# Kernel tuning notes

Hardware: AMD Instinct MI355X
Metric: run time of the kernel (lower is better)

The kernel has to match this reference:

```python
import jax, jax.numpy as jnp
import numpy as np

D_MODEL = 256; D_FFN = 1024; N_LEVELS = 4; N_HEADS = 8; N_POINTS = 4; N_VT = 8
D_HEAD = D_MODEL // N_HEADS
SHAPES = [(64, 64), (32, 32), (16, 16), (8, 8)]
L_SP = sum(h * w for h, w in SHAPES)  # 5440
BATCH = 4
EPS = 1e-5


def _ln(x, g, b):
    m = jnp.mean(x, -1, keepdims=True)
    xc = x - m
    v = jnp.mean(xc * xc, -1, keepdims=True)
    return g * xc * jax.lax.rsqrt(v + EPS) + b


def _bilinear(v_flat, x, y, H, W):
    # v_flat: (N, H*W, M, Dh); x, y: (N, Q, M) pixel coords (align_corners=False, zero padding)
    x0 = jnp.floor(x); y0 = jnp.floor(y)
    wx = x - x0; wy = y - y0
    out = 0.0
    for cx, cy, w in ((x0, y0, (1 - wx) * (1 - wy)), (x0 + 1, y0, wx * (1 - wy)),
                      (x0, y0 + 1, (1 - wx) * wy), (x0 + 1, y0 + 1, wx * wy)):
        valid = (cx >= 0) & (cx < W) & (cy >= 0) & (cy < H)
        xi = jnp.clip(cx, 0, W - 1).astype(jnp.int32)
        yi = jnp.clip(cy, 0, H - 1).astype(jnp.int32)
        idx = (yi * W + xi)[..., None]  # (N, Q, M, 1)
        g = jnp.take_along_axis(v_flat, idx, axis=1)  # (N, Q, M, Dh)
        out = out + (w * valid)[..., None] * g
    return out


def _msdeform_attn(query, ref, value_in, shapes_np, pad_mask, Wv, bv, Wo, bo, Wa, ba, Wp, bp):
    N, Lq, D = query.shape
    M, Lv, P, Dh = N_HEADS, N_LEVELS, N_POINTS, D_HEAD
    value = value_in @ Wv.T + bv
    value = jnp.where(pad_mask[..., None], 0.0, value)
    value = value.reshape(N, Lq, M, Dh)
    off = (query @ Wo.T + bo).reshape(N, Lq, M, Lv, P, 2)
    attn = jax.nn.softmax((query @ Wa.T + ba).reshape(N, Lq, M, Lv * P), axis=-1)
    attn = attn.reshape(N, Lq, M, Lv, P)
    # offset normalizer is (W, H) per level
    normalizer = jnp.asarray([[w, h] for h, w in shapes_np], jnp.float32)
    loc = ref[:, :, None, :, None, :] + off / normalizer[None, None, None, :, None, :]
    out = 0.0
    start = 0
    for l, (H, W) in enumerate(shapes_np):
        v_l = value[:, start:start + H * W]  # (N, H*W, M, Dh)
        x = (loc[:, :, :, l, :, 0] * W - 0.5).transpose(0, 1, 3, 2).reshape(N, Lq * P, M)
        y = (loc[:, :, :, l, :, 1] * H - 0.5).transpose(0, 1, 3, 2).reshape(N, Lq * P, M)
        samp = _bilinear(v_l, x, y, H, W).reshape(N, Lq, P, M, Dh)
        out = out + jnp.einsum('nqpmd,nqmp->nqmd', samp, attn[:, :, :, l, :])
        start += H * W
    return out.reshape(N, Lq, D) @ Wp.T + bp


def setup_inputs() -> dict:
    key = jax.random.key(0)
    ks = jax.random.split(key, 16)
    N, D = BATCH, D_MODEL
    Lq = L_SP + N_VT
    s = D ** -0.5
    rn = lambda k, sh, sc=1.0: jax.random.normal(k, sh, dtype=jnp.float32) * sc
    starts = np.cumsum([0] + [h * w for h, w in SHAPES[:-1]])
    return {
        'src': rn(ks[0], (N, L_SP, D)),
        'pos': rn(ks[1], (N, L_SP, D), 0.1),
        'reference_points': jax.random.uniform(ks[2], (N, Lq, N_LEVELS, 2), dtype=jnp.float32),
        'spatial_shapes': jnp.asarray(SHAPES, jnp.int32),
        'level_start_index': jnp.asarray(starts, jnp.int32),
        'padding_mask': jnp.zeros((N, Lq), bool),
        'all_vt': rn(ks[3], (N, 75 * N_VT, D)),
        'sel_vt': rn(ks[4], (N, N_VT, D)),
        'W_value': rn(ks[5], (D, D), s), 'b_value': jnp.zeros((D,), jnp.float32),
        'W_off': rn(ks[6], (N_HEADS * N_LEVELS * N_POINTS * 2, D), s),
        'b_off': rn(ks[7], (N_HEADS * N_LEVELS * N_POINTS * 2,), 0.1),
        'W_attn': rn(ks[8], (N_HEADS * N_LEVELS * N_POINTS, D), s),
        'b_attn': jnp.zeros((N_HEADS * N_LEVELS * N_POINTS,), jnp.float32),
        'W_out': rn(ks[9], (D, D), s), 'b_out': jnp.zeros((D,), jnp.float32),
        'g1': jnp.ones((D,), jnp.float32), 'beta1': jnp.zeros((D,), jnp.float32),
        'W1': rn(ks[10], (D_FFN, D), s), 'bf1': jnp.zeros((D_FFN,), jnp.float32),
        'W2': rn(ks[11], (D, D_FFN), D_FFN ** -0.5), 'bf2': jnp.zeros((D,), jnp.float32),
        'g2': jnp.ones((D,), jnp.float32), 'beta2': jnp.zeros((D,), jnp.float32),
    }


def reference(src, pos, reference_points, spatial_shapes, level_start_index, padding_mask,
              all_vt, sel_vt, W_value, b_value, W_off, b_off, W_attn, b_attn, W_out, b_out,
              g1, beta1, W1, bf1, W2, bf2, g2, beta2):
    shapes_np = [tuple(int(v) for v in row) for row in np.asarray(spatial_shapes)]
    q = jnp.concatenate([src + pos, sel_vt], axis=1)      # (N, Lq, D)
    v_in = jnp.concatenate([src, sel_vt], axis=1)
    src2 = _msdeform_attn(q, reference_points, v_in, shapes_np, padding_mask,
                          W_value, b_value, W_off, b_off, W_attn, b_attn, W_out, b_out)
    x = _ln(v_in + src2, g1, beta1)
    h = jax.nn.relu(x @ W1.T + bf1) @ W2.T + bf2
    x = _ln(x + h, g2, beta2)
    return (x[:, :L_SP, :], all_vt, x[:, L_SP:, :])
```

## Files before the change

kernel.cpp:

```cpp
#include <hip/hip_runtime.h>
#include <math.h>

#define NB   4
#define LQ   5448
#define LSP  5440
#define NR   21792
#define DM   256

typedef unsigned short u16;
typedef __attribute__((ext_vector_type(8))) short short8;
typedef __attribute__((ext_vector_type(4))) float f32x4;
typedef __attribute__((ext_vector_type(4))) unsigned int uint4v;

__device__ __forceinline__ u16 f2bf(float f) {
  unsigned int u = __float_as_uint(f);
  u = (u + 0x7fff + ((u >> 16) & 1)) >> 16;
  return (u16)u;
}
__device__ __forceinline__ float bf2f(u16 u) {
  return __uint_as_float(((unsigned int)u) << 16);
}
__device__ __forceinline__ uint4v pack8(float4 a, float4 b) {
  uint4v r;
  r.x = (unsigned)f2bf(a.x) | ((unsigned)f2bf(a.y) << 16);
  r.y = (unsigned)f2bf(a.z) | ((unsigned)f2bf(a.w) << 16);
  r.z = (unsigned)f2bf(b.x) | ((unsigned)f2bf(b.y) << 16);
  r.w = (unsigned)f2bf(b.z) | ((unsigned)f2bf(b.w) << 16);
  return r;
}

#define OFF_R0 0ull
#define OFF_R1 44630016ull
#define OFF_R2 55787520ull
#define OFF_R3 66945024ull
#define OFF_WB 78102528ull
#define OFF_BI 79609856ull

#define WOF_V  0
#define WOF_OA 65536
#define WOF_P  163840
#define WOF_1  229376
#define WOF_2  491520
#define NWELEM 753664

#define OUT0 5570560ull
#define OUT1 614400ull

__global__ __launch_bounds__(256) void convw_k(
    const float* __restrict__ Wv, const float* __restrict__ Wo,
    const float* __restrict__ Wa, const float* __restrict__ Wp,
    const float* __restrict__ W1, const float* __restrict__ W2,
    const float* __restrict__ bo, const float* __restrict__ ba,
    u16* __restrict__ out, float* __restrict__ boa,
    const float* __restrict__ avt, float* __restrict__ avt_dst)
{
  const int b = blockIdx.x;
  if (b >= NWELEM / 256) {
    const int i = (b - NWELEM / 256) * 256 + threadIdx.x;
    ((float4*)avt_dst)[i] = ((const float4*)avt)[i];
    return;
  }
  const int gid = b * 256 + threadIdx.x;
  if (gid < 384) boa[gid] = (gid < 256) ? bo[gid] : ba[gid - 256];
  float v;
  if (gid < WOF_OA) {
    v = Wv[gid];
  } else if (gid < WOF_P) {
    const int o = gid - WOF_OA;
    v = (o < 65536) ? Wo[o] : Wa[o - 65536];
  } else if (gid < WOF_1) {
    v = Wp[gid - WOF_P];
  } else if (gid < WOF_2) {
    v = W1[gid - WOF_1];
  } else {
    v = W2[gid - WOF_2];
  }
  out[gid] = f2bf(v);
}

__global__ __launch_bounds__(256) void headgemm_k(
    const float* __restrict__ src, const float* __restrict__ pos,
    const float* __restrict__ sel, const u16* __restrict__ WBp,
    const float* __restrict__ bv, const float* __restrict__ boa,
    u16* __restrict__ val_bf, float* __restrict__ oabuf)
{
  __shared__ u16 Av[32 * 256];
  __shared__ u16 Aq[32 * 256];
  __shared__ u16 Bs[4 * 4096];
  const int tid = threadIdx.x;
  const int w = tid >> 6, lane = tid & 63;
  const int l15 = lane & 15, quad = lane >> 4;
  const int m0 = blockIdx.y * 32;
  const int swz = (quad ^ ((l15 >> 1) & 3)) * 8;

  const int rA = (tid & 127) >> 2;
  const int pA = tid & 3;
  const int jb = ((tid >> 7) & 1) * 4;
  const int cA = (pA ^ ((rA >> 1) & 3)) * 8;
  const int ldsA = rA * 32 + pA * 8;
  int gmA = m0 + rA; if (gmA >= NR) gmA = NR - 1;
  const int an = gmA / LQ, ai = gmA - an * LQ;
  const float* aV; const float* aP = nullptr;
  if (ai < LSP) {
    aV = src + ((size_t)(an * LSP + ai)) * DM;
    aP = pos + ((size_t)(an * LSP + ai)) * DM;
  } else {
    aV = sel + ((size_t)(an * 8 + (ai - LSP))) * DM;
  }

#pragma unroll
  for (int i = 0; i < 4; i += 2) {
    const int j0 = jb + i, j1 = jb + i + 1;
    float4 v0a = *(const float4*)(aV + j0 * 32 + cA);
    float4 v0b = *(const float4*)(aV + j0 * 32 + cA + 4);
    float4 v1a = *(const float4*)(aV + j1 * 32 + cA);
    float4 v1b = *(const float4*)(aV + j1 * 32 + cA + 4);
    *(uint4v*)&Av[j0 * 1024 + ldsA] = pack8(v0a, v0b);
    *(uint4v*)&Av[j1 * 1024 + ldsA] = pack8(v1a, v1b);
    if (aP) {
      const float4 p0a = *(const float4*)(aP + j0 * 32 + cA);
      const float4 p0b = *(const float4*)(aP + j0 * 32 + cA + 4);
      const float4 p1a = *(const float4*)(aP + j1 * 32 + cA);
      const float4 p1b = *(const float4*)(aP + j1 * 32 + cA + 4);
      v0a.x += p0a.x; v0a.y += p0a.y; v0a.z += p0a.z; v0a.w += p0a.w;
      v0b.x += p0b.x; v0b.y += p0b.y; v0b.z += p0b.z; v0b.w += p0b.w;
      v1a.x += p1a.x; v1a.y += p1a.y; v1a.z += p1a.z; v1a.w += p1a.w;
      v1b.x += p1b.x; v1b.y += p1b.y; v1b.z += p1b.z; v1b.w += p1b.w;
    }
    *(uint4v*)&Aq[j0 * 1024 + ldsA] = pack8(v0a, v0b);
    *(uint4v*)&Aq[j1 * 1024 + ldsA] = pack8(v1a, v1b);
  }
  __syncthreads();

  int rB[4], cB[4], lB[4];
#pragma unroll
  for (int i = 0; i < 4; ++i) {
    const int g = lane + i * 64;
    rB[i] = g >> 2;
    const int p = g & 3;
    cB[i] = (p ^ ((rB[i] >> 1) & 3)) * 8;
    lB[i] = w * 4096 + rB[i] * 32 + p * 8;
  }

#pragma unroll
  for (int it = 0; it < 3; ++it) {
    const bool act = (it < 2) || (w < 2);
    const int coloff = (it == 2) ? 256 : 0;
    const u16* Brow = WBp + ((it == 0) ? WOF_V : WOF_OA)
                    + (size_t)(coloff + w * 64) * 256;
    const u16* Alds = (it == 0) ? Av : Aq;
    f32x4 acc[2][4] = {};

    if (act) {
      uint4v rb0[4], rb1[4];
#pragma unroll
      for (int i = 0; i < 4; ++i)
        rb0[i] = *(const uint4v*)(Brow + (size_t)rB[i] * 256 + cB[i]);
#pragma unroll
      for (int i = 0; i < 4; ++i)
        rb1[i] = *(const uint4v*)(Brow + (size_t)rB[i] * 256 + 32 + cB[i]);
#pragma unroll
      for (int i = 0; i < 4; ++i) *(uint4v*)&Bs[lB[i]] = rb0[i];

#pragma unroll
      for (int j = 0; j < 8; ++j) {
        if (j < 6) {
          if ((j & 1) == 0) {
#pragma unroll
            for (int i = 0; i < 4; ++i)
              rb0[i] = *(const uint4v*)(Brow + (size_t)rB[i] * 256 + (j + 2) * 32 + cB[i]);
          } else {
#pragma unroll
            for (int i = 0; i < 4; ++i)
              rb1[i] = *(const uint4v*)(Brow + (size_t)rB[i] * 256 + (j + 2) * 32 + cB[i]);
          }
        }
        short8 af[2], bfr[4];
#pragma unroll
        for (int r = 0; r < 2; ++r)
          af[r] = *(const short8*)&Alds[j * 1024 + (r * 16 + l15) * 32 + swz];
#pragma unroll
        for (int c = 0; c < 4; ++c)
          bfr[c] = *(const short8*)&Bs[w * 4096 + (j & 1) * 2048 + (c * 16 + l15) * 32 + swz];
        if (j < 7) {
          const int buf = ((j + 1) & 1) * 2048;
          if ((j & 1) == 0) {
#pragma unroll
            for (int i = 0; i < 4; ++i) *(uint4v*)&Bs[lB[i] + buf] = rb1[i];
          } else {
#pragma unroll
            for (int i = 0; i < 4; ++i) *(uint4v*)&Bs[lB[i] + buf] = rb0[i];
          }
        }
#pragma unroll
        for (int r = 0; r < 2; ++r)
#pragma unroll
          for (int c = 0; c < 4; ++c)
            acc[r][c] = __builtin_amdgcn_mfma_f32_16x16x32_bf16(af[r], bfr[c], acc[r][c], 0, 0, 0);
      }

      int col[4]; float bb[4];
#pragma unroll
      for (int c = 0; c < 4; ++c) {
        col[c] = coloff + w * 64 + c * 16 + l15;
        bb[c] = (it == 0) ? bv[col[c]] : boa[col[c]];
      }
      if (it == 0) {
#pragma unroll
        for (int c = 0; c < 4; ++c)
#pragma unroll
          for (int r = 0; r < 2; ++r)
#pragma unroll
            for (int j = 0; j < 4; ++j) {
              const int row = m0 + r * 16 + quad * 4 + j;
              if (row < NR)
                val_bf[(size_t)row * 256 + col[c]] = f2bf(acc[r][c][j] + bb[c]);
            }
      } else {
#pragma unroll
        for (int c = 0; c < 4; ++c)
#pragma unroll
          for (int r = 0; r < 2; ++r)
#pragma unroll
            for (int j = 0; j < 4; ++j) {
              const int row = m0 + r * 16 + quad * 4 + j;
              if (row < NR)
                oabuf[(size_t)row * 384 + col[c]] = acc[r][c][j] + bb[c];
            }
      }
    }
  }
}

template <int AMODE, int EPI, int BN, int NITER>
__global__ __launch_bounds__(BN) void gemmP(
    const u16* __restrict__ A, int lda,
    const float* __restrict__ src, const float* __restrict__ pos,
    const float* __restrict__ sel,
    const u16* __restrict__ B, int ldb,
    const float* __restrict__ bias, int K,
    u16* __restrict__ outb, int ldob,
    const u16* __restrict__ xbf,
    const float* __restrict__ gvec, const float* __restrict__ bvec,
    float* __restrict__ outf, int ldof)
{
  constexpr int NW = BN / 64;
  __shared__ u16 As[32 * 256];
  __shared__ u16 Bs[NW * 4096];
  const int tid = threadIdx.x;
  const int w = tid >> 6, lane = tid & 63;
  const int l15 = lane & 15, quad = lane >> 4;
  const int m0 = blockIdx.y * 32;
  const int n0 = blockIdx.x * (BN * NITER);
  const int swz = (quad ^ ((l15 >> 1) & 3)) * 8;

  const int rA = (tid & 127) >> 2;
  const int pA = tid & 3;
  const int jb = ((tid >> 7) & 1) * 4;
  const int cA = (pA ^ ((rA >> 1) & 3)) * 8;
  const int ldsA = rA * 32 + pA * 8;
  int gmA = m0 + rA; if (gmA >= NR) gmA = NR - 1;
  const float* aV = nullptr; const float* aP = nullptr;
  if (AMODE) {
    const int n = gmA / LQ, i = gmA - n * LQ;
    if (i < LSP) {
      aV = src + ((size_t)(n * LSP + i)) * DM;
      if (AMODE == 1) aP = pos + ((size_t)(n * LSP + i)) * DM;
    } else {
      aV = sel + ((size_t)(n * 8 + (i - LSP))) * DM;
    }
  }

  int rB[4], cB[4], lB[4];
#pragma unroll
  for (int i = 0; i < 4; ++i) {
    const int g = lane + i * 64;
    rB[i] = g >> 2;
    const int p = g & 3;
    cB[i] = (p ^ ((rB[i] >> 1) & 3)) * 8;
    lB[i] = w * 4096 + rB[i] * 32 + p * 8;
  }

  for (int it = 0; it < NITER; ++it) {
    const u16* Brow = B + (size_t)(n0 + it * BN + w * 64) * ldb;
    f32x4 acc[2][4] = {};

    for (int kc = 0; kc < K; kc += 256) {
      if (NITER == 1 || it == 0) {
        if (kc) __syncthreads();
        if (tid < 256) {
          if (AMODE == 0) {
            const u16* ap = A + (size_t)gmA * lda + kc + cA;
            uint4v t0 = *(const uint4v*)(ap + (jb + 0) * 32);
            uint4v t1 = *(const uint4v*)(ap + (jb + 1) * 32);
            uint4v t2 = *(const uint4v*)(ap + (jb + 2) * 32);
            uint4v t3 = *(const uint4v*)(ap + (jb + 3) * 32);
            *(uint4v*)&As[(jb + 0) * 1024 + ldsA] = t0;
            *(uint4v*)&As[(jb + 1) * 1024 + ldsA] = t1;
            *(uint4v*)&As[(jb + 2) * 1024 + ldsA] = t2;
            *(uint4v*)&As[(jb + 3) * 1024 + ldsA] = t3;
          } else {
#pragma unroll
            for (int i = 0; i < 4; i += 2) {
              const int j0 = jb + i, j1 = jb + i + 1;
              float4 v0a = *(const float4*)(aV + kc + j0 * 32 + cA);
              float4 v0b = *(const float4*)(aV + kc + j0 * 32 + cA + 4);
              float4 v1a = *(const float4*)(aV + kc + j1 * 32 + cA);
              float4 v1b = *(const float4*)(aV + kc + j1 * 32 + cA + 4);
              if (AMODE == 1 && aP) {
                const float4 p0a = *(const float4*)(aP + kc + j0 * 32 + cA);
                const float4 p0b = *(const float4*)(aP + kc + j0 * 32 + cA + 4);
                const float4 p1a = *(const float4*)(aP + kc + j1 * 32 + cA);
                const float4 p1b = *(const float4*)(aP + kc + j1 * 32 + cA + 4);
                v0a.x += p0a.x; v0a.y += p0a.y; v0a.z += p0a.z; v0a.w += p0a.w;
                v0b.x += p0b.x; v0b.y += p0b.y; v0b.z += p0b.z; v0b.w += p0b.w;
                v1a.x += p1a.x; v1a.y += p1a.y; v1a.z += p1a.z; v1a.w += p1a.w;
                v1b.x += p1b.x; v1b.y += p1b.y; v1b.z += p1b.z; v1b.w += p1b.w;
              }
              *(uint4v*)&As[j0 * 1024 + ldsA] = pack8(v0a, v0b);
              *(uint4v*)&As[j1 * 1024 + ldsA] = pack8(v1a, v1b);
            }
          }
        }
        __syncthreads();
      }

      uint4v rb0[4], rb1[4];
#pragma unroll
      for (int i = 0; i < 4; ++i)
        rb0[i] = *(const uint4v*)(Brow + (size_t)rB[i] * ldb + kc + cB[i]);
#pragma unroll
      for (int i = 0; i < 4; ++i)
        rb1[i] = *(const uint4v*)(Brow + (size_t)rB[i] * ldb + kc + 32 + cB[i]);
#pragma unroll
      for (int i = 0; i < 4; ++i) *(uint4v*)&Bs[lB[i]] = rb0[i];

#pragma unroll
      for (int j = 0; j < 8; ++j) {
        if (j < 6) {
          if ((j & 1) == 0) {
#pragma unroll
            for (int i = 0; i < 4; ++i)
              rb0[i] = *(const uint4v*)(Brow + (size_t)rB[i] * ldb + kc + (j + 2) * 32 + cB[i]);
          } else {
#pragma unroll
            for (int i = 0; i < 4; ++i)
              rb1[i] = *(const uint4v*)(Brow + (size_t)rB[i] * ldb + kc + (j + 2) * 32 + cB[i]);
          }
        }
        short8 af[2], bfr[4];
#pragma unroll
        for (int r = 0; r < 2; ++r)
          af[r] = *(const short8*)&As[j * 1024 + (r * 16 + l15) * 32 + swz];
#pragma unroll
        for (int c = 0; c < 4; ++c)
          bfr[c] = *(const short8*)&Bs[w * 4096 + (j & 1) * 2048 + (c * 16 + l15) * 32 + swz];
        if (j < 7) {
          const int buf = ((j + 1) & 1) * 2048;
          if ((j & 1) == 0) {
#pragma unroll
            for (int i = 0; i < 4; ++i) *(uint4v*)&Bs[lB[i] + buf] = rb1[i];
          } else {
#pragma unroll
            for (int i = 0; i < 4; ++i) *(uint4v*)&Bs[lB[i] + buf] = rb0[i];
          }
        }
#pragma unroll
        for (int r = 0; r < 2; ++r)
#pragma unroll
          for (int c = 0; c < 4; ++c)
            acc[r][c] = __builtin_amdgcn_mfma_f32_16x16x32_bf16(af[r], bfr[c], acc[r][c], 0, 0, 0);
      }
    }

    int col[4];
    float bb[4];
#pragma unroll
    for (int c = 0; c < 4; ++c) {
      col[c] = n0 + it * BN + w * 64 + c * 16 + l15;
      bb[c] = bias[col[c]];
    }

    if (EPI == 4) {
#pragma unroll
      for (int c = 0; c < 4; ++c)
#pragma unroll
        for (int r = 0; r < 2; ++r)
#pragma unroll
          for (int j = 0; j < 4; ++j) {
            const int row = m0 + r * 16 + quad * 4 + j;
            if (row < NR) outf[(size_t)row * ldof + col[c]] = acc[r][c][j] + bb[c];
          }
      continue;
    }

    if (EPI <= 1) {
#pragma unroll
      for (int c = 0; c < 4; ++c)
#pragma unroll
        for (int r = 0; r < 2; ++r)
#pragma unroll
          for (int j = 0; j < 4; ++j) {
            const int row = m0 + r * 16 + quad * 4 + j;
            if (row < NR) {
              float v = acc[r][c][j] + bb[c];
              if (EPI == 1) v = fmaxf(v, 0.f);
              outb[(size_t)row * ldob + col[c]] = f2bf(v);
            }
          }
      continue;
    }

    __syncthreads();
    float sv[2][4], sq[2][4];
#pragma unroll
    for (int r = 0; r < 2; ++r) {
#pragma unroll
      for (int j = 0; j < 4; ++j) {
        const int row = m0 + r * 16 + quad * 4 + j;
        const int rc = (row < NR) ? row : NR - 1;
        if (EPI == 2) {
          const int n = rc / LQ;
          const int i = rc - n * LQ;
          const float* resb = (i < LSP)
              ? src + ((size_t)(n * LSP + i)) * DM
              : sel + ((size_t)(n * 8 + (i - LSP))) * DM;
#pragma unroll
          for (int c = 0; c < 4; ++c) acc[r][c][j] += bb[c] + resb[col[c]];
        } else {
#pragma unroll
          for (int c = 0; c < 4; ++c)
            acc[r][c][j] += bb[c] + bf2f(xbf[(size_t)rc * DM + col[c]]);
        }
        float s = 0.f, q = 0.f;
#pragma unroll
        for (int c = 0; c < 4; ++c) {
          const float v = acc[r][c][j];
          s += v; q += v * v;
        }
        sv[r][j] = s; sq[r][j] = q;
      }
    }
#pragma unroll
    for (int off = 1; off < 16; off <<= 1) {
#pragma unroll
      for (int r = 0; r < 2; ++r)
#pragma unroll
        for (int j = 0; j < 4; ++j) {
          sv[r][j] += __shfl_xor(sv[r][j], off, 64);
          sq[r][j] += __shfl_xor(sq[r][j], off, 64);
        }
    }
    float* red = (float*)As;
    if (l15 == 0) {
#pragma unroll
      for (int r = 0; r < 2; ++r)
#pragma unroll
        for (int j = 0; j < 4; ++j) {
          const int rl = r * 16 + quad * 4 + j;
          red[(rl * 4 + w) * 2 + 0] = sv[r][j];
          red[(rl * 4 + w) * 2 + 1] = sq[r][j];
        }
    }
    __syncthreads();

    float gg[4], b2[4];
#pragma unroll
    for (int c = 0; c < 4; ++c) { gg[c] = gvec[col[c]]; b2[c] = bvec[col[c]]; }

#pragma unroll
    for (int r = 0; r < 2; ++r) {
#pragma unroll
      for (int j = 0; j < 4; ++j) {
        const int row = m0 + r * 16 + quad * 4 + j;
        if (row >= NR) continue;
        const int rl = r * 16 + quad * 4 + j;
        float ms = 0.f, mq = 0.f;
#pragma unroll
        for (int ww = 0; ww < 4; ++ww) {
          ms += red[(rl * 4 + ww) * 2 + 0];
          mq += red[(rl * 4 + ww) * 2 + 1];
        }
        const float mean = ms * (1.f / 256.f);
        const float var = mq * (1.f / 256.f) - mean * mean;
        const float rin = rsqrtf(var + 1e-5f);
        if (EPI == 2) {
#pragma unroll
          for (int c = 0; c < 4; ++c)
            outb[(size_t)row * DM + col[c]] =
                f2bf(gg[c] * (acc[r][c][j] - mean) * rin + b2[c]);
        } else {
          const int n = row / LQ;
          const int i = row - n * LQ;
          float* dst = (i < LSP)
              ? outf + (size_t)(n * LSP + i) * DM
              : outf + OUT0 + OUT1 + (size_t)(n * 8 + (i - LSP)) * DM;
#pragma unroll
          for (int c = 0; c < 4; ++c)
            dst[col[c]] = gg[c] * (acc[r][c][j] - mean) * rin + b2[c];
        }
      }
    }
  }
}

__device__ __forceinline__ void fma8(float* a, const uint4v u, float w) {
  a[0] += w * __uint_as_float(u.x << 16);
  a[1] += w * __uint_as_float(u.x & 0xffff0000u);
  a[2] += w * __uint_as_float(u.y << 16);
  a[3] += w * __uint_as_float(u.y & 0xffff0000u);
  a[4] += w * __uint_as_float(u.z << 16);
  a[5] += w * __uint_as_float(u.z & 0xffff0000u);
  a[6] += w * __uint_as_float(u.w << 16);
  a[7] += w * __uint_as_float(u.w & 0xffff0000u);
}

__global__ __launch_bounds__(256) void sample4_k(
    const u16* __restrict__ value, const float* __restrict__ oa,
    const float* __restrict__ ref, u16* __restrict__ samp)
{
  const int lb = blockIdx.x;
  const int xcd = lb & 7;
  const int idx = lb >> 3;
  const int batch = xcd >> 1;
  const int rg = idx * 2 + (xcd & 1);
  const int lane = threadIdx.x & 63;
  const int hi = lane >> 5;
  const int li = lane & 31;
  const int m = li >> 2, q4 = li & 3;
  const int row = batch * LQ + rg * 4 + (threadIdx.x >> 6);

  const float* oar = oa + (size_t)row * 384;
  const float* offm = oar + m * 32;

  const float4 lg = *(const float4*)(oar + 256 + m * 16 + q4 * 4);
  float mx = fmaxf(fmaxf(lg.x, lg.y), fmaxf(lg.z, lg.w));
  mx = fmaxf(mx, __shfl_xor(mx, 1, 64));
  mx = fmaxf(mx, __shfl_xor(mx, 2, 64));
  const float e0 = __expf(lg.x - mx), e1 = __expf(lg.y - mx),
              e2 = __expf(lg.z - mx), e3 = __expf(lg.w - mx);
  float s = e0 + e1 + e2 + e3;
  s += __shfl_xor(s, 1, 64);
  s += __shfl_xor(s, 2, 64);
  const float inv = 1.f / s;
  float wp[4] = {e0 * inv, e1 * inv, e2 * inv, e3 * inv};

  const int L0 = hi * 2;
  float aw[2][4];
#pragma unroll
  for (int p = 0; p < 4; ++p) {
#pragma unroll
    for (int t = 0; t < 2; ++t)
      aw[t][p] = __shfl(wp[p], (lane & ~3) | (L0 + t), 64);
  }

  const float4 r01 = *(const float4*)(ref + (size_t)row * 8);
  const float4 r23 = *(const float4*)(ref + (size_t)row * 8 + 4);
  const float RXa[4] = {r01.x, r01.z, r23.x, r23.z};
  const float RYa[4] = {r01.y, r01.w, r23.y, r23.w};
  const int HW[4] = {64, 32, 16, 8};
  const int ST[4] = {0, 4096, 5120, 5376};

  float a[8] = {};
#pragma unroll
  for (int t = 0; t < 2; ++t) {
    const int l = L0 + t;
    const int W = HW[l];
    const float rx = RXa[l], ry = RYa[l];
    const u16* vb = value + ((size_t)(batch * LQ + ST[l])) * DM + m * 32 + q4 * 8;
    const float4 oA = *(const float4*)(offm + l * 8);
    const float4 oB = *(const float4*)(offm + l * 8 + 4);
    const float ox[4] = {oA.x, oA.z, oB.x, oB.z};
    const float oy[4] = {oA.y, oA.w, oB.y, oB.w};
#pragma unroll
    for (int p = 0; p < 4; ++p) {
      const float px = rx * (float)W + ox[p] - 0.5f;
      const float py = ry * (float)W + oy[p] - 0.5f;
      const float xf = floorf(px), yf = floorf(py);
      const float wx = px - xf, wy = py - yf;
      const int x0 = (int)xf, y0 = (int)yf;
      const int x1 = x0 + 1, y1 = y0 + 1;
      const float vx0 = ((x0 >= 0) & (x0 < W)) ? 1.f : 0.f;
      const float vx1 = ((x1 >= 0) & (x1 < W)) ? 1.f : 0.f;
      const float vy0 = ((y0 >= 0) & (y0 < W)) ? 1.f : 0.f;
      const float vy1 = ((y1 >= 0) & (y1 < W)) ? 1.f : 0.f;
      const int cx0 = min(max(x0, 0), W - 1), cx1 = min(max(x1, 0), W - 1);
      const int cy0 = min(max(y0, 0), W - 1), cy1 = min(max(y1, 0), W - 1);
      const float awp = aw[t][p];
      const float w00 = awp * (1.f - wx) * (1.f - wy) * vx0 * vy0;
      const float w01 = awp * wx * (1.f - wy) * vx1 * vy0;
      const float w10 = awp * (1.f - wx) * wy * vx0 * vy1;
      const float w11 = awp * wx * wy * vx1 * vy1;
      const uint4v v00 = *(const uint4v*)(vb + (size_t)(cy0 * W + cx0) * DM);
      const uint4v v01 = *(const uint4v*)(vb + (size_t)(cy0 * W + cx1) * DM);
      const uint4v v10 = *(const uint4v*)(vb + (size_t)(cy1 * W + cx0) * DM);
      const uint4v v11 = *(const uint4v*)(vb + (size_t)(cy1 * W + cx1) * DM);
      fma8(a, v00, w00);
      fma8(a, v01, w01);
      fma8(a, v10, w10);
      fma8(a, v11, w11);
    }
  }
#pragma unroll
  for (int i = 0; i < 8; ++i) a[i] += __shfl_xor(a[i], 32, 64);

  if (hi == 0) {
    uint4v ov;
    ov.x = (unsigned int)f2bf(a[0]) | ((unsigned int)f2bf(a[1]) << 16);
    ov.y = (unsigned int)f2bf(a[2]) | ((unsigned int)f2bf(a[3]) << 16);
    ov.z = (unsigned int)f2bf(a[4]) | ((unsigned int)f2bf(a[5]) << 16);
    ov.w = (unsigned int)f2bf(a[6]) | ((unsigned int)f2bf(a[7]) << 16);
    *(uint4v*)(samp + (size_t)row * DM + m * 32 + q4 * 8) = ov;
  }
}

extern "C" void kernel_launch(void* const* d_in, const int* in_sizes, int n_in,
                              void* d_out, int out_size, void* d_ws, size_t ws_size,
                              hipStream_t stream)
{
  const float* src = (const float*)d_in[0];
  const float* pos = (const float*)d_in[1];
  const float* ref = (const float*)d_in[2];
  const float* all_vt = (const float*)d_in[6];
  const float* sel = (const float*)d_in[7];
  const float* Wv = (const float*)d_in[8];
  const float* bv = (const float*)d_in[9];
  const float* Wo = (const float*)d_in[10];
  const float* bo = (const float*)d_in[11];
  const float* Wa = (const float*)d_in[12];
  const float* ba = (const float*)d_in[13];
  const float* Wp = (const float*)d_in[14];
  const float* bp = (const float*)d_in[15];
  const float* g1 = (const float*)d_in[16];
  const float* be1 = (const float*)d_in[17];
  const float* W1 = (const float*)d_in[18];
  const float* b1 = (const float*)d_in[19];
  const float* W2 = (const float*)d_in[20];
  const float* b2 = (const float*)d_in[21];
  const float* g2 = (const float*)d_in[22];
  const float* be2 = (const float*)d_in[23];

  char* ws = (char*)d_ws;
  float* oabuf = (float*)(ws + OFF_R0);
  u16* h_bf    = (u16*)(ws + OFF_R0);
  u16* samp_bf = (u16*)(ws + OFF_R1);
  u16* x_bf    = (u16*)(ws + OFF_R2);
  u16* val_bf  = (u16*)(ws + OFF_R3);
  u16* WB      = (u16*)(ws + OFF_WB);
  float* boa   = (float*)(ws + OFF_BI);

  const dim3 b256(256);
  const int MT32 = (NR + 31) / 32;

  convw_k<<<dim3(NWELEM / 256 + 600), b256, 0, stream>>>(
      Wv, Wo, Wa, Wp, W1, W2, bo, ba, WB, boa,
      all_vt, (float*)d_out + OUT0);
  headgemm_k<<<dim3(1, MT32), b256, 0, stream>>>(
      src, pos, sel, WB, bv, boa, val_bf, oabuf);
  sample4_k<<<dim3(8 * 681), b256, 0, stream>>>(val_bf, oabuf, ref, samp_bf);
  gemmP<0, 2, 256, 1><<<dim3(1, MT32), b256, 0, stream>>>(
      samp_bf, 256, src, nullptr, sel, WB + WOF_P, 256, bp, 256,
      x_bf, 256, nullptr, g1, be1, nullptr, 0);
  gemmP<0, 1, 256, 4><<<dim3(1, MT32), b256, 0, stream>>>(
      x_bf, 256, nullptr, nullptr, nullptr, WB + WOF_1, 256, b1, 256,
      h_bf, 1024, nullptr, nullptr, nullptr, nullptr, 0);
  gemmP<0, 3, 256, 1><<<dim3(1, MT32), b256, 0, stream>>>(
      h_bf, 1024, nullptr, nullptr, nullptr, WB + WOF_2, 1024, b2, 1024,
      nullptr, 0, x_bf, g2, be2, (float*)d_out, 0);
}
```

Baseline: 275.8 us.

## Load B-operand MFMA fragments directly from global memory, bypassing LDS

```diff
diff --git a/kernel.cpp b/kernel.cpp
--- a/kernel.cpp
+++ b/kernel.cpp
@@ -11,6 +11,8 @@
 typedef __attribute__((ext_vector_type(8))) short short8;
 typedef __attribute__((ext_vector_type(4))) float f32x4;
 typedef __attribute__((ext_vector_type(4))) unsigned int uint4v;
+
+#define MFMA(d, a, b) d = __builtin_amdgcn_mfma_f32_16x16x32_bf16(a, b, d, 0, 0, 0)
 
 __device__ __forceinline__ u16 f2bf(float f) {
   unsigned int u = __float_as_uint(f);
@@ -78,6 +80,20 @@
   out[gid] = f2bf(v);
 }
 
+#define JSTEP(J, BUF)                                                        \
+  {                                                                          \
+    const short8 af0 = *(const short8*)&As[(J) * 1024 + l15 * 32 + swz];     \
+    const short8 af1 = *(const short8*)&As[(J) * 1024 + (16 + l15) * 32 + swz]; \
+    _Pragma("unroll") for (int c = 0; c < 4; ++c) {                          \
+      MFMA(acc[0][c], af0, BUF[c]);                                          \
+      MFMA(acc[1][c], af1, BUF[c]);                                          \
+    }                                                                        \
+    if ((J) + 4 < 8) {                                                       \
+      _Pragma("unroll") for (int c = 0; c < 4; ++c)                          \
+        BUF[c] = *(const short8*)(bpc[c] + kc + ((J) + 4) * 32);             \
+    }                                                                        \
+  }
+
 __global__ __launch_bounds__(256) void headgemm_k(
     const float* __restrict__ src, const float* __restrict__ pos,
     const float* __restrict__ sel, const u16* __restrict__ WBp,
@@ -86,7 +102,6 @@
 {
   __shared__ u16 Av[32 * 256];
   __shared__ u16 Aq[32 * 256];
-  __shared__ u16 Bs[4 * 4096];
   const int tid = threadIdx.x;
   const int w = tid >> 6, lane = tid & 63;
   const int l15 = lane & 15, quad = lane >> 4;
@@ -132,72 +147,31 @@
   }
   __syncthreads();
 
-  int rB[4], cB[4], lB[4];
-#pragma unroll
-  for (int i = 0; i < 4; ++i) {
-    const int g = lane + i * 64;
-    rB[i] = g >> 2;
-    const int p = g & 3;
-    cB[i] = (p ^ ((rB[i] >> 1) & 3)) * 8;
-    lB[i] = w * 4096 + rB[i] * 32 + p * 8;
-  }
-
 #pragma unroll
   for (int it = 0; it < 3; ++it) {
     const bool act = (it < 2) || (w < 2);
     const int coloff = (it == 2) ? 256 : 0;
-    const u16* Brow = WBp + ((it == 0) ? WOF_V : WOF_OA)
-                    + (size_t)(coloff + w * 64) * 256;
-    const u16* Alds = (it == 0) ? Av : Aq;
+    const u16* As = (it == 0) ? Av : Aq;
     f32x4 acc[2][4] = {};
 
     if (act) {
-      uint4v rb0[4], rb1[4];
-#pragma unroll
-      for (int i = 0; i < 4; ++i)
-        rb0[i] = *(const uint4v*)(Brow + (size_t)rB[i] * 256 + cB[i]);
-#pragma unroll
-      for (int i = 0; i < 4; ++i)
-        rb1[i] = *(const uint4v*)(Brow + (size_t)rB[i] * 256 + 32 + cB[i]);
-#pragma unroll
-      for (int i = 0; i < 4; ++i) *(uint4v*)&Bs[lB[i]] = rb0[i];
-
-#pragma unroll
-      for (int j = 0; j < 8; ++j) {
-        if (j < 6) {
-          if ((j & 1) == 0) {
-#pragma unroll
-            for (int i = 0; i < 4; ++i)
-              rb0[i] = *(const uint4v*)(Brow + (size_t)rB[i] * 256 + (j + 2) * 32 + cB[i]);
-          } else {
-#pragma unroll
-            for (int i = 0; i < 4; ++i)
-              rb1[i] = *(const uint4v*)(Brow + (size_t)rB[i] * 256 + (j + 2) * 32 + cB[i]);
-          }
-        }
-        short8 af[2], bfr[4];
-#pragma unroll
-        for (int r = 0; r < 2; ++r)
-          af[r] = *(const short8*)&Alds[j * 1024 + (r * 16 + l15) * 32 + swz];
-#pragma unroll
-        for (int c = 0; c < 4; ++c)
-          bfr[c] = *(const short8*)&Bs[w * 4096 + (j & 1) * 2048 + (c * 16 + l15) * 32 + swz];
-        if (j < 7) {
-          const int buf = ((j + 1) & 1) * 2048;
-          if ((j & 1) == 0) {
-#pragma unroll
-            for (int i = 0; i < 4; ++i) *(uint4v*)&Bs[lB[i] + buf] = rb1[i];
-          } else {
-#pragma unroll
-            for (int i = 0; i < 4; ++i) *(uint4v*)&Bs[lB[i] + buf] = rb0[i];
-          }
-        }
-#pragma unroll
-        for (int r = 0; r < 2; ++r)
-#pragma unroll
-          for (int c = 0; c < 4; ++c)
-            acc[r][c] = __builtin_amdgcn_mfma_f32_16x16x32_bf16(af[r], bfr[c], acc[r][c], 0, 0, 0);
-      }
+      const u16* bpc[4];
+#pragma unroll
+      for (int c = 0; c < 4; ++c)
+        bpc[c] = WBp + ((it == 0) ? WOF_V : WOF_OA)
+               + (size_t)(coloff + w * 64 + c * 16 + l15) * 256 + quad * 8;
+      const int kc = 0;
+      short8 b0[4], b1[4], b2[4], b3[4];
+#pragma unroll
+      for (int c = 0; c < 4; ++c) b0[c] = *(const short8*)(bpc[c] + 0 * 32);
+#pragma unroll
+      for (int c = 0; c < 4; ++c) b1[c] = *(const short8*)(bpc[c] + 1 * 32);
+#pragma unroll
+      for (int c = 0; c < 4; ++c) b2[c] = *(const short8*)(bpc[c] + 2 * 32);
+#pragma unroll
+      for (int c = 0; c < 4; ++c) b3[c] = *(const short8*)(bpc[c] + 3 * 32);
+      JSTEP(0, b0) JSTEP(1, b1) JSTEP(2, b2) JSTEP(3, b3)
+      JSTEP(4, b0) JSTEP(5, b1) JSTEP(6, b2) JSTEP(7, b3)
 
       int col[4]; float bb[4];
 #pragma unroll
@@ -244,9 +218,7 @@
     const float* __restrict__ gvec, const float* __restrict__ bvec,
     float* __restrict__ outf, int ldof)
 {
-  constexpr int NW = BN / 64;
   __shared__ u16 As[32 * 256];
-  __shared__ u16 Bs[NW * 4096];
   const int tid = threadIdx.x;
   const int w = tid >> 6, lane = tid & 63;
   const int l15 = lane & 15, quad = lane >> 4;
@@ -271,18 +243,11 @@
     }
   }
 
-  int rB[4], cB[4], lB[4];
-#pragma unroll
-  for (int i = 0; i < 4; ++i) {
-    const int g = lane + i * 64;
-    rB[i] = g >> 2;
-    const int p = g & 3;
-    cB[i] = (p ^ ((rB[i] >> 1) & 3)) * 8;
-    lB[i] = w * 4096 + rB[i] * 32 + p * 8;
-  }
-
   for (int it = 0; it < NITER; ++it) {
-    const u16* Brow = B + (size_t)(n0 + it * BN + w * 64) * ldb;
+    const u16* bpc[4];
+#pragma unroll
+    for (int c = 0; c < 4; ++c)
+      bpc[c] = B + (size_t)(n0 + it * BN + w * 64 + c * 16 + l15) * ldb + quad * 8;
     f32x4 acc[2][4] = {};
 
     for (int kc = 0; kc < K; kc += 256) {
@@ -325,52 +290,17 @@
         __syncthreads();
       }
 
-      uint4v rb0[4], rb1[4];
-#pragma unroll
-      for (int i = 0; i < 4; ++i)
-        rb0[i] = *(const uint4v*)(Brow + (size_t)rB[i] * ldb + kc + cB[i]);
-#pragma unroll
-      for (int i = 0; i < 4; ++i)
-        rb1[i] = *(const uint4v*)(Brow + (size_t)rB[i] * ldb + kc + 32 + cB[i]);
-#pragma unroll
-      for (int i = 0; i < 4; ++i) *(uint4v*)&Bs[lB[i]] = rb0[i];
-
-#pragma unroll
-      for (int j = 0; j < 8; ++j) {
-        if (j < 6) {
-          if ((j & 1) == 0) {
-#pragma unroll
-            for (int i = 0; i < 4; ++i)
-              rb0[i] = *(const uint4v*)(Brow + (size_t)rB[i] * ldb + kc + (j + 2) * 32 + cB[i]);
-          } else {
-#pragma unroll
-            for (int i = 0; i < 4; ++i)
-              rb1[i] = *(const uint4v*)(Brow + (size_t)rB[i] * ldb + kc + (j + 2) * 32 + cB[i]);
-          }
-        }
-        short8 af[2], bfr[4];
-#pragma unroll
-        for (int r = 0; r < 2; ++r)
-          af[r] = *(const short8*)&As[j * 1024 + (r * 16 + l15) * 32 + swz];
-#pragma unroll
-        for (int c = 0; c < 4; ++c)
-          bfr[c] = *(const short8*)&Bs[w * 4096 + (j & 1) * 2048 + (c * 16 + l15) * 32 + swz];
-        if (j < 7) {
-          const int buf = ((j + 1) & 1) * 2048;
-          if ((j & 1) == 0) {
-#pragma unroll
-            for (int i = 0; i < 4; ++i) *(uint4v*)&Bs[lB[i] + buf] = rb1[i];
-          } else {
-#pragma unroll
-            for (int i = 0; i < 4; ++i) *(uint4v*)&Bs[lB[i] + buf] = rb0[i];
-          }
-        }
-#pragma unroll
-        for (int r = 0; r < 2; ++r)
-#pragma unroll
-          for (int c = 0; c < 4; ++c)
-            acc[r][c] = __builtin_amdgcn_mfma_f32_16x16x32_bf16(af[r], bfr[c], acc[r][c], 0, 0, 0);
-      }
+      short8 b0[4], b1[4], b2[4], b3[4];
+#pragma unroll
+      for (int c = 0; c < 4; ++c) b0[c] = *(const short8*)(bpc[c] + kc + 0 * 32);
+#pragma unroll
+      for (int c = 0; c < 4; ++c) b1[c] = *(const short8*)(bpc[c] + kc + 1 * 32);
+#pragma unroll
+      for (int c = 0; c < 4; ++c) b2[c] = *(const short8*)(bpc[c] + kc + 2 * 32);
+#pragma unroll
+      for (int c = 0; c < 4; ++c) b3[c] = *(const short8*)(bpc[c] + kc + 3 * 32);
+      JSTEP(0, b0) JSTEP(1, b1) JSTEP(2, b2) JSTEP(3, b3)
+      JSTEP(4, b0) JSTEP(5, b1) JSTEP(6, b2) JSTEP(7, b3)
     }
 
     int col[4];
@@ -464,9 +394,9 @@
     }
     __syncthreads();
 
-    float gg[4], b2[4];
-#pragma unroll
-    for (int c = 0; c < 4; ++c) { gg[c] = gvec[col[c]]; b2[c] = bvec[col[c]]; }
+    float gg[4], b2v[4];
+#pragma unroll
+    for (int c = 0; c < 4; ++c) { gg[c] = gvec[col[c]]; b2v[c] = bvec[col[c]]; }
 
 #pragma unroll
     for (int r = 0; r < 2; ++r) {
@@ -488,7 +418,7 @@
 #pragma unroll
           for (int c = 0; c < 4; ++c)
             outb[(size_t)row * DM + col[c]] =
-                f2bf(gg[c] * (acc[r][c][j] - mean) * rin + b2[c]);
+                f2bf(gg[c] * (acc[r][c][j] - mean) * rin + b2v[c]);
         } else {
           const int n = row / LQ;
           const int i = row - n * LQ;
@@ -497,7 +427,7 @@
               : outf + OUT0 + OUT1 + (size_t)(n * 8 + (i - LSP)) * DM;
 #pragma unroll
           for (int c = 0; c < 4; ++c)
-            dst[col[c]] = gg[c] * (acc[r][c][j] - mean) * rin + b2[c];
+            dst[col[c]] = gg[c] * (acc[r][c][j] - mean) * rin + b2v[c];
         }
       }
     }
```

Result: slower. 340.7 us (+23.5%).
